# Performance work log

Measured on AMD Instinct MI355X. Metric: run time of the kernel, lower is better.

## Reference

```python
import jax, jax.numpy as jnp
import numpy as np


def _dwconv(x, w, pad, dil=1):
    # x: [B,C,H,W], w: [C,1,kh,kw] depthwise
    C = x.shape[1]
    return jax.lax.conv_general_dilated(
        x, w, window_strides=(1, 1), padding=[(pad, pad), (pad, pad)],
        rhs_dilation=(dil, dil),
        dimension_numbers=('NCHW', 'OIHW', 'NCHW'),
        feature_group_count=C)


def _conv1x1(x, w, b):
    # w: [O,C,1,1]
    return jnp.einsum('bchw,oc->bohw', x, w[:, :, 0, 0]) + b[None, :, None, None]


def _ln(x, g, b, eps=1e-6):
    mu = x.mean(-1, keepdims=True)
    var = ((x - mu) ** 2).mean(-1, keepdims=True)
    return (x - mu) * jax.lax.rsqrt(var + eps) * g + b


def _gelu(x):
    return jax.nn.gelu(x, approximate=False)  # torch nn.GELU default = exact erf


def _starts(h, step, ps):
    s = []
    for i in range(0, h + step - ps, step):
        s.append(i if i + ps <= h else h - ps)
    return np.asarray(s, np.int32)


def _divisor(h, w, step, ps):
    # replicates patch_reverse's overlap /2 strips exactly
    div = np.ones((h, w), np.float32)
    for i in range(step, h + step - ps, step):
        top, down = i, i + ps - step
        if top + ps > h:
            top = h - ps
        div[top:down, :] *= 2.0
    for j in range(step, w + step - ps, step):
        left, right = j, j + ps - step
        if left + ps > w:
            left = w - ps
        div[:, left:right] *= 2.0
    return div


def _forward(x, ps, lth_dw_w, lth_pw_w, lth_pw_b, lth_gate_w, lth_gate_b, lth_scale,
             ln1_g, ln1_b, ln2_g, ln2_b, qkv_w, gate_w, gate_b, proj_w, pe_w, pe_b,
             fc1_w, fc1_b, dw_w, dw_b, fc2_w, fc2_b):
    B, C, H, W = x.shape
    step = ps - 2
    # ---- Low_to_high ----
    low = x.reshape(B, C, H // 2, 2, W // 2, 2).mean(axis=(3, 5))  # adaptive avg pool (even H,W)
    low_up = jax.image.resize(low, (B, C, H, W), method='bilinear')  # align_corners=False
    hf = x - low_up
    sgate = jax.nn.sigmoid(_conv1x1(jnp.abs(hf), lth_gate_w, lth_gate_b))  # [B,1,H,W]
    refined = _conv1x1(_gelu(_dwconv(hf, lth_dw_w, pad=2, dil=2)), lth_pw_w, lth_pw_b)
    x = x + lth_scale * refined * sgate
    # ---- patch_divide (overlapping windows) ----
    st = ps if (H == ps and W == ps) else step
    tops, lefts = _starts(H, st, ps), _starts(W, st, ps)
    nh, nw = len(tops), len(lefts)
    r = tops[:, None] + np.arange(ps)   # [nh, ps]
    c = lefts[:, None] + np.arange(ps)  # [nw, ps]
    crop = x[:, :, r[:, None, :, None], c[None, :, None, :]]  # [B,C,nh,nw,ps,ps]
    t = crop.transpose(0, 2, 3, 4, 5, 1).reshape(B * nh * nw, ps * ps, C)  # (b n) (h w) c
    # ---- Attention (single-head, qk_dim == dim) ----
    y = _ln(t, ln1_g, ln1_b)
    qkv = y @ qkv_w                      # [Bn, N, 3C]
    q, k, v = jnp.split(qkv, 3, axis=-1)
    z = _gelu(y @ gate_w + gate_b)       # gate
    qimg = q.transpose(0, 2, 1).reshape(-1, C, ps, ps)
    pe = (_dwconv(qimg, pe_w, pad=1) + pe_b[None, :, None, None])
    pe = pe.reshape(-1, C, ps * ps).transpose(0, 2, 1)
    scale = C ** (-0.5)                  # qk_dim = dim = C
    attn = jax.nn.softmax(jnp.einsum('bnc,bmc->bnm', q, k) * scale, axis=-1)
    out = jnp.einsum('bnm,bmc->bnc', attn, v) + pe
    t = (out * z) @ proj_w + t           # proj + residual
    # ---- patch_reverse (overlap-add, strips averaged) ----
    crop = t.reshape(B, nh, nw, ps, ps, C).transpose(0, 5, 1, 2, 3, 4)  # [B,C,nh,nw,ps,ps]
    summed = jnp.zeros_like(x).at[:, :, r[:, None, :, None], c[None, :, None, :]].add(crop)
    x = summed * (1.0 / jnp.asarray(_divisor(H, W, st, ps)))
    # ---- ConvFFN ----
    xt = x.reshape(B, C, H * W).transpose(0, 2, 1)  # [B,HW,C]
    y = _ln(xt, ln2_g, ln2_b)
    y = _gelu(y @ fc1_w + fc1_b)                    # [B,HW,2C]
    yimg = y.transpose(0, 2, 1).reshape(B, -1, H, W)
    y = y + (_dwconv(yimg, dw_w, pad=2) + dw_b[None, :, None, None]).reshape(B, -1, H * W).transpose(0, 2, 1)
    y = y @ fc2_w + fc2_b
    xt = y + xt
    return xt.transpose(0, 2, 1).reshape(B, C, H, W)


def setup_inputs() -> dict:
    key = jax.random.key(0)
    ks = jax.random.split(key, 16)
    B, C, H, W = 8, 128, 128, 128
    HID = 2 * C
    def w(i, shape, s=0.02):
        return jax.random.normal(ks[i], shape, jnp.float32) * s
    return {
        'x': jax.random.normal(ks[0], (B, C, H, W), jnp.float32),
        'ps': 16,
        'lth_dw_w': w(1, (C, 1, 3, 3), 0.1),
        'lth_pw_w': w(2, (C, C, 1, 1)),
        'lth_pw_b': jnp.zeros((C,), jnp.float32),
        'lth_gate_w': w(3, (1, C, 1, 1), 0.1),
        'lth_gate_b': jnp.zeros((1,), jnp.float32),
        'lth_scale': w(4, (1, C, 1, 1), 0.1),
        'ln1_g': jnp.ones((C,), jnp.float32),
        'ln1_b': jnp.zeros((C,), jnp.float32),
        'ln2_g': jnp.ones((C,), jnp.float32),
        'ln2_b': jnp.zeros((C,), jnp.float32),
        'qkv_w': w(5, (C, 3 * C)),
        'gate_w': w(6, (C, C)),
        'gate_b': jnp.zeros((C,), jnp.float32),
        'proj_w': w(7, (C, C)),
        'pe_w': w(8, (C, 1, 3, 3), 0.1),
        'pe_b': jnp.zeros((C,), jnp.float32),
        'fc1_w': w(9, (C, HID)),
        'fc1_b': jnp.zeros((HID,), jnp.float32),
        'dw_w': w(10, (HID, 1, 5, 5), 0.1),
        'dw_b': jnp.zeros((HID,), jnp.float32),
        'fc2_w': w(11, (HID, C)),
        'fc2_b': jnp.zeros((C,), jnp.float32),
    }


def reference(x, ps, lth_dw_w, lth_pw_w, lth_pw_b, lth_gate_w, lth_gate_b, lth_scale,
              ln1_g, ln1_b, ln2_g, ln2_b, qkv_w, gate_w, gate_b, proj_w, pe_w, pe_b,
              fc1_w, fc1_b, dw_w, dw_b, fc2_w, fc2_b):
    return _forward(x, ps, lth_dw_w, lth_pw_w, lth_pw_b, lth_gate_w, lth_gate_b, lth_scale,
                    ln1_g, ln1_b, ln2_g, ln2_b, qkv_w, gate_w, gate_b, proj_w, pe_w, pe_b,
                    fc1_w, fc1_b, dw_w, dw_b, fc2_w, fc2_b)
```

## Files before the change

### kernel.cpp

```cpp
#include <hip/hip_runtime.h>
#include <hip/hip_bf16.h>
#include <math.h>

typedef __hip_bfloat16 bf16;
typedef __attribute__((ext_vector_type(8))) short bf16x8;
typedef __attribute__((ext_vector_type(4))) float f32x4;

static constexpr int B_ = 8, C_ = 128, H_ = 128, W_ = 128;
static constexpr int N_ = H_ * W_;
static constexpr int NWIN = 648;

__device__ __forceinline__ float b2f(bf16 v) { return __bfloat162float(v); }
__device__ __forceinline__ bf16 f2b(float v) { return __float2bfloat16(v); }

__device__ __forceinline__ float gelu_f(float x) {
    float xs = x * 0.70710678118654752f;
    float ax = fabsf(xs);
    float t = 1.0f / fmaf(0.3275911f, ax, 1.0f);
    float poly = t * fmaf(t, fmaf(t, fmaf(t, fmaf(t, 1.061405429f, -1.453152027f), 1.421413741f), -0.284496736f), 0.254829592f);
    float erf_ax = fmaf(-poly, __expf(-ax * ax), 1.0f);
    float erfv = copysignf(erf_ax, xs);
    return 0.5f * x * (1.0f + erfv);
}

__device__ __forceinline__ void load_row12(const char* tile, int a, int wg, float* dst) {
    int base = a * 288 + wg * 16;
    union { uint4 u; bf16 hh[8]; } c0, c1, c2;
    c0.u = *(const uint4*)(tile + base);
    c1.u = *(const uint4*)(tile + base + 16);
    c2.u = *(const uint4*)(tile + base + 32);
    dst[0] = b2f(c0.hh[6]); dst[1] = b2f(c0.hh[7]);
    #pragma unroll
    for (int j = 0; j < 8; ++j) dst[2 + j] = b2f(c1.hh[j]);
    dst[10] = b2f(c2.hh[0]); dst[11] = b2f(c2.hh[1]);
}

__global__ __launch_bounds__(256) void k_wprep(const float* __restrict__ projw, const float* __restrict__ qkvw,
                                               const float* __restrict__ gatew, const float* __restrict__ w1,
                                               const float* __restrict__ w2, const float* __restrict__ pww,
                                               bf16* __restrict__ wt, bf16* __restrict__ wqkv,
                                               bf16* __restrict__ wt1, bf16* __restrict__ wt2,
                                               bf16* __restrict__ wpw) {
    int idx = blockIdx.x * 256 + threadIdx.x;
    if (idx < 16384) {
        int o = idx >> 7, c = idx & 127;
        wt[idx] = f2b(projw[c * 128 + o]);
    } else if (idx < 81920) {
        int i = idx - 16384; int o = i >> 7, c = i & 127;
        wqkv[i] = f2b((o < 384) ? qkvw[c * 384 + o] : gatew[c * 128 + (o - 384)]);
    } else if (idx < 114688) {
        int i = idx - 81920; int o = i >> 7, c = i & 127;
        wt1[i] = f2b(w1[c * 256 + o]);
    } else if (idx < 147456) {
        int i = idx - 114688; int o = i >> 8, c = i & 255;
        wt2[i] = f2b(w2[c * 128 + o]);
    } else {
        int i = idx - 147456;
        wpw[i] = f2b(pww[i]);
    }
}

__global__ __launch_bounds__(256) void k_hf2(const float* __restrict__ x, bf16* __restrict__ hf) {
    __shared__ float lowt[10][64];
    int tid = threadIdx.x;
    int bid = blockIdx.x;
    int ht = bid & 7, c = (bid >> 3) & 127, b = bid >> 10;
    const float* xp = x + (size_t)(b * C_ + c) * N_;
    int h0 = ht * 16;
    int lo0 = (h0 >> 1) - 1;
    for (int e = tid; e < 640; e += 256) {
        int lr = e >> 6, jc = e & 63;
        int j = lo0 + lr; j = j < 0 ? 0 : (j > 63 ? 63 : j);
        const float* pr = xp + (2 * j) * W_ + 2 * jc;
        lowt[lr][jc] = (pr[0] + pr[1] + pr[W_] + pr[W_ + 1]) * 0.25f;
    }
    __syncthreads();
    int hl = tid >> 4, wg = tid & 15;
    int h = h0 + hl;
    int jh = h >> 1;
    int j0, j1; float wh0, wh1;
    if (h & 1) { j0 = jh; j1 = jh + 1 > 63 ? 63 : jh + 1; wh0 = 0.75f; wh1 = 0.25f; }
    else       { j0 = jh - 1 < 0 ? 0 : jh - 1; j1 = jh;   wh0 = 0.25f; wh1 = 0.75f; }
    int l0 = j0 - lo0, l1 = j1 - lo0;
    float4 xa = *(const float4*)(xp + h * W_ + wg * 8);
    float4 xb = *(const float4*)(xp + h * W_ + wg * 8 + 4);
    float xv[8] = {xa.x, xa.y, xa.z, xa.w, xb.x, xb.y, xb.z, xb.w};
    union { bf16 hh[8]; uint4 u; } outv;
    #pragma unroll
    for (int k2 = 0; k2 < 8; ++k2) {
        int w = wg * 8 + k2;
        int jw = w >> 1;
        int w0, w1; float ww0, ww1;
        if (w & 1) { w0 = jw; w1 = jw + 1 > 63 ? 63 : jw + 1; ww0 = 0.75f; ww1 = 0.25f; }
        else       { w0 = jw - 1 < 0 ? 0 : jw - 1; w1 = jw;   ww0 = 0.25f; ww1 = 0.75f; }
        float up = wh0 * (ww0 * lowt[l0][w0] + ww1 * lowt[l0][w1])
                 + wh1 * (ww0 * lowt[l1][w0] + ww1 * lowt[l1][w1]);
        outv.hh[k2] = f2b(xv[k2] - up);
    }
    *(uint4*)(hf + (size_t)(b * C_ + c) * N_ + h * W_ + wg * 8) = outv.u;
}

__global__ __launch_bounds__(256) void k_sgate(const bf16* __restrict__ hf, const float* __restrict__ gw,
                                               const float* __restrict__ gb, float* __restrict__ sg) {
    int idx = blockIdx.x * 256 + threadIdx.x;
    int n = idx & (N_ - 1); int b = idx >> 14;
    const bf16* p = hf + (size_t)b * C_ * N_ + n;
    float s = 0.f;
    for (int c = 0; c < C_; ++c) s += gw[c] * fabsf(b2f(p[(size_t)c * N_]));
    s += gb[0];
    sg[idx] = 1.0f / (1.0f + __expf(-s));
}

__global__ __launch_bounds__(256) void k_dw3p(const bf16* __restrict__ hf, const float* __restrict__ wdw,
                                              bf16* __restrict__ g) {
    __shared__ __align__(16) char tile[38016];
    int tid = threadIdx.x;
    int bid = blockIdx.x;
    int ch = bid & 127, b = bid >> 7;
    const bf16* p = hf + (size_t)(b * C_ + ch) * N_;
    for (int e = tid; e < 2376; e += 256) *(uint4*)(tile + e * 16) = (uint4){0, 0, 0, 0};
    __syncthreads();
    for (int e = tid; e < 2048; e += 256) {
        int gr = e >> 4, slot = e & 15;
        uint4 val = *(const uint4*)(p + gr * 128 + slot * 8);
        *(uint4*)(tile + (gr + 2) * 288 + 16 + slot * 16) = val;
    }
    float kw[9];
    #pragma unroll
    for (int j = 0; j < 9; ++j) kw[j] = wdw[ch * 9 + j];
    __syncthreads();
    int hg = tid >> 4, wg = tid & 15;
    int h0 = hg * 8;
    float ring[5][12];
    #pragma unroll
    for (int j = 0; j < 4; ++j) load_row12(tile, h0 + j, wg, ring[j]);
    bf16* op = g + (size_t)(b * C_ + ch) * N_;
    #pragma unroll
    for (int rr = 0; rr < 8; ++rr) {
        load_row12(tile, h0 + rr + 4, wg, ring[(rr + 4) % 5]);
        float acc[8] = {};
        #pragma unroll
        for (int ky = 0; ky < 3; ++ky) {
            const float* e = ring[(rr + 2 * ky) % 5];
            #pragma unroll
            for (int ow = 0; ow < 8; ++ow) {
                acc[ow] = fmaf(kw[ky * 3 + 0], e[ow], acc[ow]);
                acc[ow] = fmaf(kw[ky * 3 + 1], e[ow + 2], acc[ow]);
                acc[ow] = fmaf(kw[ky * 3 + 2], e[ow + 4], acc[ow]);
            }
        }
        union { bf16 h[8]; uint4 u; } outv;
        #pragma unroll
        for (int ow = 0; ow < 8; ++ow) outv.h[ow] = f2b(gelu_f(acc[ow]));
        *(uint4*)(op + (h0 + rr) * 128 + wg * 8) = outv.u;
    }
}

__global__ __launch_bounds__(256) void k_pw_mfma(const bf16* __restrict__ g, const bf16* __restrict__ wpw,
                                                 const float* __restrict__ pwb, const float* __restrict__ x,
                                                 const float* __restrict__ scale, const float* __restrict__ sg,
                                                 bf16* __restrict__ x1) {
    __shared__ __align__(16) char lds[49152];
    int tid = threadIdx.x;
    int lane = tid & 63, w = tid >> 6;
    int l15 = lane & 15, lhi = lane >> 4;
    int gtok = blockIdx.x * 64; int b = gtok >> 14; int nb = gtok & (N_ - 1);
    char* wch = lds + 16384;
    for (int e = tid; e < 8192; e += 256) {
        int c = e >> 6, i = e & 63;
        bf16 val = g[(size_t)(b * C_ + c) * N_ + nb + i];
        *(bf16*)(lds + i * 256 + ((2 * c) ^ ((i & 7) << 4))) = val;
    }
    for (int e = tid; e < 2048; e += 256) {
        int row = e >> 4, slot = e & 15;
        uint4 val = *(const uint4*)((const char*)wpw + row * 256 + slot * 16);
        *(uint4*)(wch + row * 256 + ((slot * 16) ^ ((row & 7) << 4))) = val;
    }
    __syncthreads();
    bf16x8 afr[4];
    {
        int row = w * 16 + l15;
        #pragma unroll
        for (int cc = 0; cc < 4; ++cc) {
            int cbyt = cc * 64 + lhi * 16;
            afr[cc] = *(const bf16x8*)(lds + row * 256 + (cbyt ^ ((row & 7) << 4)));
        }
    }
    f32x4 acc[8];
    #pragma unroll
    for (int t = 0; t < 8; ++t) acc[t] = (f32x4){0.f, 0.f, 0.f, 0.f};
    #pragma unroll
    for (int ot = 0; ot < 8; ++ot) {
        int row = ot * 16 + l15;
        #pragma unroll
        for (int cc = 0; cc < 4; ++cc) {
            int cbyt = cc * 64 + lhi * 16;
            bf16x8 bfr = *(const bf16x8*)(wch + row * 256 + (cbyt ^ ((row & 7) << 4)));
            acc[ot] = __builtin_amdgcn_mfma_f32_16x16x32_bf16(afr[cc], bfr, acc[ot], 0, 0, 0);
        }
    }
    int n0 = nb + w * 16 + lhi * 4;
    float4 sg4 = *(const float4*)&sg[b * N_ + n0];
    #pragma unroll
    for (int ot = 0; ot < 8; ++ot) {
        int o = ot * 16 + l15;
        size_t obase = (size_t)(b * C_ + o) * N_ + n0;
        float4 x4 = *(const float4*)&x[obase];
        float sc = scale[o], bi = pwb[o];
        union { bf16 h[4]; uint2 u; } t4;
        t4.h[0] = f2b(x4.x + sc * (acc[ot][0] + bi) * sg4.x);
        t4.h[1] = f2b(x4.y + sc * (acc[ot][1] + bi) * sg4.y);
        t4.h[2] = f2b(x4.z + sc * (acc[ot][2] + bi) * sg4.z);
        t4.h[3] = f2b(x4.w + sc * (acc[ot][3] + bi) * sg4.w);
        *(uint2*)(x1 + obase) = t4.u;
    }
}

__global__ __launch_bounds__(256) void k_qkv_mfma(const bf16* __restrict__ x1, const float* __restrict__ lng,
                                                  const float* __restrict__ lnb, const bf16* __restrict__ wall,
                                                  const float* __restrict__ gateb,
                                                  bf16* __restrict__ q, bf16* __restrict__ k,
                                                  bf16* __restrict__ v, bf16* __restrict__ z) {
    __shared__ __align__(16) char lds[49664];
    __shared__ float red2[8][64];
    __shared__ float mu_l[64], rs_l[64];
    int tid = threadIdx.x;
    int lane = tid & 63, w = tid >> 6;
    int l15 = lane & 15, lhi = lane >> 4;
    int win = blockIdx.x >> 2; int qbase = (blockIdx.x & 3) * 64;
    int b = win / 81; int r0 = win % 81; int top = (r0 / 9) * 14, left = (r0 % 9) * 14;
    float* xf = (float*)(lds + 16384);
    char* wchunk = lds + 16384;
    for (int e = tid; e < 8192; e += 256) {
        int c = e >> 6, i = e & 63; int tok = qbase + i; int p = tok >> 4, qq = tok & 15;
        xf[c * 65 + i] = b2f(x1[(size_t)(b * C_ + c) * N_ + (top + p) * W_ + (left + qq)]);
    }
    __syncthreads();
    {
        int i = tid & 63, r = tid >> 6;
        float s = 0.f, ss = 0.f;
        for (int cc = r * 32; cc < r * 32 + 32; ++cc) { float vv = xf[cc * 65 + i]; s += vv; ss += vv * vv; }
        red2[r][i] = s; red2[4 + r][i] = ss;
    }
    __syncthreads();
    if (tid < 64) {
        float s = red2[0][tid] + red2[1][tid] + red2[2][tid] + red2[3][tid];
        float ss = red2[4][tid] + red2[5][tid] + red2[6][tid] + red2[7][tid];
        float mu = s * (1.f / 128.f); float var = ss * (1.f / 128.f) - mu * mu;
        mu_l[tid] = mu; rs_l[tid] = rsqrtf(var + 1e-6f);
    }
    __syncthreads();
    {
        int c = tid & 127;
        float g = lng[c], be = lnb[c];
        for (int e = tid; e < 8192; e += 256) {
            int i = e >> 7;
            float val = (xf[c * 65 + i] - mu_l[i]) * rs_l[i] * g + be;
            *(bf16*)(lds + i * 256 + ((2 * c) ^ ((i & 7) << 4))) = f2b(val);
        }
    }
    __syncthreads();
    bf16x8 afr[4];
    {
        int row = w * 16 + l15;
        #pragma unroll
        for (int cc = 0; cc < 4; ++cc) {
            int cbyt = cc * 64 + lhi * 16;
            afr[cc] = *(const bf16x8*)(lds + row * 256 + (cbyt ^ ((row & 7) << 4)));
        }
    }
    for (int pass = 0; pass < 4; ++pass) {
        __syncthreads();
        for (int e = tid; e < 2048; e += 256) {
            int row = e >> 4, slot = e & 15;
            uint4 val = *(const uint4*)((const char*)wall + (size_t)(pass * 128 + row) * 256 + slot * 16);
            *(uint4*)(wchunk + row * 256 + ((slot * 16) ^ ((row & 7) << 4))) = val;
        }
        __syncthreads();
        f32x4 acc[8];
        #pragma unroll
        for (int t = 0; t < 8; ++t) acc[t] = (f32x4){0.f, 0.f, 0.f, 0.f};
        #pragma unroll
        for (int ot = 0; ot < 8; ++ot) {
            int row = ot * 16 + l15;
            #pragma unroll
            for (int cc = 0; cc < 4; ++cc) {
                int cbyt = cc * 64 + lhi * 16;
                bf16x8 bfr = *(const bf16x8*)(wchunk + row * 256 + (cbyt ^ ((row & 7) << 4)));
                acc[ot] = __builtin_amdgcn_mfma_f32_16x16x32_bf16(afr[cc], bfr, acc[ot], 0, 0, 0);
            }
        }
        if (pass != 2) {
            bf16* outp = (pass == 0) ? q : (pass == 1) ? k : z;
            bool gel = (pass == 3);
            #pragma unroll
            for (int ot = 0; ot < 8; ++ot) {
                int o = ot * 16 + l15;
                float gb = gel ? gateb[o] : 0.f;
                #pragma unroll
                for (int r = 0; r < 4; ++r) {
                    int gtok = qbase + w * 16 + lhi * 4 + r;
                    float vv = acc[ot][r];
                    outp[((size_t)win * 256 + gtok) * 128 + o] = gel ? f2b(gelu_f(vv + gb)) : f2b(vv);
                }
            }
        } else {
            #pragma unroll
            for (int ot = 0; ot < 8; ++ot) {
                int o = ot * 16 + l15;
                union { bf16 h[4]; uint2 u; } t4;
                #pragma unroll
                for (int r = 0; r < 4; ++r) t4.h[r] = f2b(acc[ot][r]);
                *(uint2*)(v + (size_t)win * 32768 + (size_t)o * 256 + qbase + w * 16 + lhi * 4) = t4.u;
            }
        }
    }
}

__global__ __launch_bounds__(256) void k_attn_mfma(const bf16* __restrict__ qb, const bf16* __restrict__ kb,
                                                   const bf16* __restrict__ vb, bf16* __restrict__ ob) {
    __shared__ __align__(16) char lds[49152];
    int tid = threadIdx.x;
    int lane = tid & 63, w = tid >> 6;
    int l15 = lane & 15, lhi = lane >> 4;
    int win = blockIdx.x >> 2, qbase = (blockIdx.x & 3) * 64;
    const bf16* qg = qb + ((size_t)win * 256 + qbase) * 128;
    const bf16* kg = kb + (size_t)win * 256 * 128;
    const bf16* vg = vb + (size_t)win * 128 * 256;
    char* chunk = lds + 32768;
    for (int e = tid; e < 1024; e += 256) {
        int row = e >> 4, slot = e & 15;
        uint4 val = *(const uint4*)((const char*)qg + row * 256 + slot * 16);
        *(uint4*)(lds + row * 256 + ((slot * 16) ^ ((row & 7) << 4))) = val;
    }
    __syncthreads();
    bf16x8 afr[4];
    {
        int row = w * 16 + l15;
        #pragma unroll
        for (int cc = 0; cc < 4; ++cc) {
            int cb = cc * 64 + lhi * 16;
            afr[cc] = *(const bf16x8*)(lds + row * 256 + (cb ^ ((row & 7) << 4)));
        }
    }
    f32x4 acc[16];
    #pragma unroll
    for (int t = 0; t < 16; ++t) acc[t] = (f32x4){0.f, 0.f, 0.f, 0.f};
    for (int kc = 0; kc < 4; ++kc) {
        __syncthreads();
        for (int e = tid; e < 1024; e += 256) {
            int row = e >> 4, slot = e & 15;
            uint4 val = *(const uint4*)((const char*)kg + (size_t)(kc * 64 + row) * 256 + slot * 16);
            *(uint4*)(chunk + row * 256 + ((slot * 16) ^ ((row & 7) << 4))) = val;
        }
        __syncthreads();
        #pragma unroll
        for (int t = 0; t < 4; ++t) {
            int row = t * 16 + l15;
            #pragma unroll
            for (int cc = 0; cc < 4; ++cc) {
                int cb = cc * 64 + lhi * 16;
                bf16x8 bfr = *(const bf16x8*)(chunk + row * 256 + (cb ^ ((row & 7) << 4)));
                acc[kc * 4 + t] = __builtin_amdgcn_mfma_f32_16x16x32_bf16(afr[cc], bfr, acc[kc * 4 + t], 0, 0, 0);
            }
        }
    }
    const float sm_scale = 0.08838834764831845f;
    #pragma unroll
    for (int r = 0; r < 4; ++r) {
        float m = -1e30f;
        #pragma unroll
        for (int t = 0; t < 16; ++t) m = fmaxf(m, acc[t][r]);
        #pragma unroll
        for (int d2 = 1; d2 < 16; d2 <<= 1) m = fmaxf(m, __shfl_xor(m, d2, 64));
        float ssum = 0.f;
        #pragma unroll
        for (int t = 0; t < 16; ++t) { float p = __expf((acc[t][r] - m) * sm_scale); acc[t][r] = p; ssum += p; }
        #pragma unroll
        for (int d2 = 1; d2 < 16; d2 <<= 1) ssum += __shfl_xor(ssum, d2, 64);
        float inv = 1.f / ssum;
        #pragma unroll
        for (int t = 0; t < 16; ++t) acc[t][r] *= inv;
    }
    #pragma unroll
    for (int t = 0; t < 16; ++t) {
        #pragma unroll
        for (int r = 0; r < 4; ++r) {
            int row = w * 16 + lhi * 4 + r;
            int cb = (t * 16 + l15) * 2;
            *(bf16*)(lds + row * 512 + (cb ^ ((row & 7) << 4))) = f2b(acc[t][r]);
        }
    }
    f32x4 oacc[8];
    #pragma unroll
    for (int t = 0; t < 8; ++t) oacc[t] = (f32x4){0.f, 0.f, 0.f, 0.f};
    for (int vc = 0; vc < 4; ++vc) {
        __syncthreads();
        for (int e = tid; e < 1024; e += 256) {
            int row = e >> 3, slot = e & 7;
            uint4 val = *(const uint4*)((const char*)vg + (size_t)row * 512 + vc * 128 + slot * 16);
            *(uint4*)(chunk + row * 128 + ((slot * 16) ^ ((row & 7) << 4))) = val;
        }
        __syncthreads();
        #pragma unroll
        for (int jc = 0; jc < 2; ++jc) {
            int prow = w * 16 + l15;
            int pcb = vc * 128 + jc * 64 + lhi * 16;
            bf16x8 ap = *(const bf16x8*)(lds + prow * 512 + (pcb ^ ((prow & 7) << 4)));
            #pragma unroll
            for (int ct = 0; ct < 8; ++ct) {
                int vrow = ct * 16 + l15;
                int vcb = jc * 64 + lhi * 16;
                bf16x8 bv = *(const bf16x8*)(chunk + vrow * 128 + (vcb ^ ((vrow & 7) << 4)));
                oacc[ct] = __builtin_amdgcn_mfma_f32_16x16x32_bf16(ap, bv, oacc[ct], 0, 0, 0);
            }
        }
    }
    bf16* og = ob + ((size_t)win * 256 + qbase) * 128;
    #pragma unroll
    for (int ct = 0; ct < 8; ++ct) {
        #pragma unroll
        for (int r = 0; r < 4; ++r) {
            int row = w * 16 + lhi * 4 + r;
            og[row * 128 + ct * 16 + l15] = f2b(oacc[ct][r]);
        }
    }
}

__global__ __launch_bounds__(256) void k_peg(bf16* __restrict__ ob, const bf16* __restrict__ qb,
                                             const bf16* __restrict__ zb,
                                             const float* __restrict__ pew, const float* __restrict__ peb) {
    __shared__ float pw_lds[1152];
    __shared__ float pb_lds[128];
    int tid = threadIdx.x;
    for (int e = tid; e < 1152; e += 256) pw_lds[e] = pew[e];
    if (tid < 128) pb_lds[tid] = peb[tid];
    __syncthreads();
    int g = blockIdx.x * 256 + tid;
    int c8 = g & 15, tok = (g >> 4) & 255, win = g >> 12;
    int cb = c8 * 8;
    int pp = tok >> 4, qq = tok & 15;
    size_t base = ((size_t)win * 256 + tok) * 128 + cb;
    float pv[8];
    #pragma unroll
    for (int cc = 0; cc < 8; ++cc) pv[cc] = pb_lds[cb + cc];
    #pragma unroll
    for (int ky = 0; ky < 3; ++ky) {
        int py = pp + ky - 1; if ((unsigned)py >= 16u) continue;
        #pragma unroll
        for (int kx = 0; kx < 3; ++kx) {
            int qx = qq + kx - 1; if ((unsigned)qx >= 16u) continue;
            union { uint4 u; bf16 h[8]; } qu;
            qu.u = *(const uint4*)(qb + ((size_t)win * 256 + py * 16 + qx) * 128 + cb);
            #pragma unroll
            for (int cc = 0; cc < 8; ++cc)
                pv[cc] += pw_lds[(cb + cc) * 9 + ky * 3 + kx] * b2f(qu.h[cc]);
        }
    }
    union { uint4 u; bf16 h[8]; } ou, zu, ru;
    ou.u = *(const uint4*)(ob + base);
    zu.u = *(const uint4*)(zb + base);
    #pragma unroll
    for (int cc = 0; cc < 8; ++cc)
        ru.h[cc] = f2b((b2f(ou.h[cc]) + pv[cc]) * b2f(zu.h[cc]));
    *(uint4*)(ob + base) = ru.u;
}

__global__ __launch_bounds__(256) void k_proj(const bf16* __restrict__ ub, const bf16* __restrict__ wt,
                                              const bf16* __restrict__ x1, bf16* __restrict__ t2) {
    __shared__ __align__(16) char lds[49152];
    int tid = threadIdx.x;
    int lane = tid & 63, w = tid >> 6;
    int l15 = lane & 15, lhi = lane >> 4;
    int win = blockIdx.x >> 2, qbase = (blockIdx.x & 3) * 64;
    int b = win / 81; int r0 = win % 81; int top = (r0 / 9) * 14, left = (r0 % 9) * 14;
    const bf16* ug = ub + ((size_t)win * 256 + qbase) * 128;
    char* wchunk = lds + 16384;
    for (int e = tid; e < 1024; e += 256) {
        int row = e >> 4, slot = e & 15;
        uint4 val = *(const uint4*)((const char*)ug + row * 256 + slot * 16);
        *(uint4*)(lds + row * 256 + ((slot * 16) ^ ((row & 7) << 4))) = val;
    }
    for (int e = tid; e < 2048; e += 256) {
        int row = e >> 4, slot = e & 15;
        uint4 val = *(const uint4*)((const char*)wt + row * 256 + slot * 16);
        *(uint4*)(wchunk + row * 256 + ((slot * 16) ^ ((row & 7) << 4))) = val;
    }
    __syncthreads();
    bf16x8 afr[4];
    {
        int row = w * 16 + l15;
        #pragma unroll
        for (int cc = 0; cc < 4; ++cc) {
            int cbyt = cc * 64 + lhi * 16;
            afr[cc] = *(const bf16x8*)(lds + row * 256 + (cbyt ^ ((row & 7) << 4)));
        }
    }
    f32x4 acc[8];
    #pragma unroll
    for (int t = 0; t < 8; ++t) acc[t] = (f32x4){0.f, 0.f, 0.f, 0.f};
    #pragma unroll
    for (int ot = 0; ot < 8; ++ot) {
        int row = ot * 16 + l15;
        #pragma unroll
        for (int cc = 0; cc < 4; ++cc) {
            int cbyt = cc * 64 + lhi * 16;
            bf16x8 bfr = *(const bf16x8*)(wchunk + row * 256 + (cbyt ^ ((row & 7) << 4)));
            acc[ot] = __builtin_amdgcn_mfma_f32_16x16x32_bf16(afr[cc], bfr, acc[ot], 0, 0, 0);
        }
    }
    #pragma unroll
    for (int ot = 0; ot < 8; ++ot) {
        #pragma unroll
        for (int r = 0; r < 4; ++r) {
            int tok = w * 16 + lhi * 4 + r;
            int o = ot * 16 + l15;
            int gtok = qbase + tok;
            int p = gtok >> 4, qq = gtok & 15;
            float res = b2f(x1[(size_t)(b * C_ + o) * N_ + (top + p) * W_ + (left + qq)]);
            t2[(size_t)win * 32768 + (size_t)o * 256 + gtok] = f2b(acc[ot][r] + res);
        }
    }
}

__global__ __launch_bounds__(256) void k_fc1ln(const bf16* __restrict__ t2, const float* __restrict__ lng,
                                               const float* __restrict__ lnb, const bf16* __restrict__ wt1,
                                               const float* __restrict__ b1, bf16* __restrict__ h1,
                                               bf16* __restrict__ x2w) {
    __shared__ __align__(16) char lds[49664];
    __shared__ float red2[8][64];
    __shared__ float mu_l[64], rs_l[64];
    int tid = threadIdx.x;
    int lane = tid & 63, w = tid >> 6;
    int l15 = lane & 15, lhi = lane >> 4;
    int gtok = blockIdx.x * 64; int b = gtok >> 14; int nb = gtok & (N_ - 1);
    int h = nb >> 7, w0 = nb & 127;
    int imin = (h < 16) ? 0 : (h - 2) / 14; int imax = h / 14; if (imax > 8) imax = 8;
    int jmin0 = (w0 < 16) ? 0 : (w0 - 2) / 14;
    int jmax0 = (w0 + 63) / 14; if (jmax0 > 8) jmax0 = 8;
    float* xf = (float*)(lds + 16384);
    char* wch = lds + 16384;
    for (int e = tid; e < 8320; e += 256) xf[e] = 0.f;
    __syncthreads();
    {
        int c = tid >> 1, half = tid & 1;
        for (int ii = imin; ii <= imax; ++ii) {
            int trow = h - ii * 14;
            for (int jj = jmin0; jj <= jmax0; ++jj) {
                int s = jj * 14 - w0 + half * 8;
                if (s >= 0 && s <= 56) {
                    const bf16* tp = t2 + (size_t)((b * 9 + ii) * 9 + jj) * 32768
                                   + (size_t)c * 256 + trow * 16 + half * 8;
                    union { uint4 u; bf16 hh[8]; } qv;
                    qv.u = *(const uint4*)tp;
                    float* xr = xf + c * 65 + s;
                    #pragma unroll
                    for (int k2 = 0; k2 < 8; ++k2) xr[k2] += b2f(qv.hh[k2]);
                }
            }
        }
    }
    __syncthreads();
    for (int e = tid; e < 2048; e += 256) {
        int c = e >> 4, qd = e & 15;
        int i0 = qd * 4;
        union { bf16 hh[4]; uint2 u; } t4;
        #pragma unroll
        for (int k2 = 0; k2 < 4; ++k2) {
            int i = i0 + k2;
            int wp = w0 + i;
            int jmn = (wp < 16) ? 0 : (wp - 2) / 14; int jmx = wp / 14; if (jmx > 8) jmx = 8;
            float inv = 1.0f / (float)((imax - imin + 1) * (jmx - jmn + 1));
            float val = xf[c * 65 + i] * inv;
            xf[c * 65 + i] = val;
            t4.hh[k2] = f2b(val);
        }
        *(uint2*)(x2w + (size_t)(b * C_ + c) * N_ + nb + i0) = t4.u;
    }
    __syncthreads();
    {
        int i = tid & 63, r = tid >> 6;
        float s = 0.f, ss = 0.f;
        for (int cc = r * 32; cc < r * 32 + 32; ++cc) { float vv = xf[cc * 65 + i]; s += vv; ss += vv * vv; }
        red2[r][i] = s; red2[4 + r][i] = ss;
    }
    __syncthreads();
    if (tid < 64) {
        float s = red2[0][tid] + red2[1][tid] + red2[2][tid] + red2[3][tid];
        float ss = red2[4][tid] + red2[5][tid] + red2[6][tid] + red2[7][tid];
        float mu = s * (1.f / 128.f); float var = ss * (1.f / 128.f) - mu * mu;
        mu_l[tid] = mu; rs_l[tid] = rsqrtf(var + 1e-6f);
    }
    __syncthreads();
    {
        int c = tid & 127;
        float g = lng[c], be = lnb[c];
        for (int e = tid; e < 8192; e += 256) {
            int i = e >> 7;
            float val = (xf[c * 65 + i] - mu_l[i]) * rs_l[i] * g + be;
            *(bf16*)(lds + i * 256 + ((2 * c) ^ ((i & 7) << 4))) = f2b(val);
        }
    }
    __syncthreads();
    bf16x8 afr[4];
    {
        int row = w * 16 + l15;
        #pragma unroll
        for (int cc = 0; cc < 4; ++cc) {
            int cbyt = cc * 64 + lhi * 16;
            afr[cc] = *(const bf16x8*)(lds + row * 256 + (cbyt ^ ((row & 7) << 4)));
        }
    }
    for (int p = 0; p < 2; ++p) {
        __syncthreads();
        for (int e = tid; e < 2048; e += 256) {
            int row = e >> 4, slot = e & 15;
            uint4 val = *(const uint4*)((const char*)wt1 + (size_t)(p * 128 + row) * 256 + slot * 16);
            *(uint4*)(wch + row * 256 + ((slot * 16) ^ ((row & 7) << 4))) = val;
        }
        __syncthreads();
        f32x4 acc[8];
        #pragma unroll
        for (int t = 0; t < 8; ++t) acc[t] = (f32x4){0.f, 0.f, 0.f, 0.f};
        #pragma unroll
        for (int ot = 0; ot < 8; ++ot) {
            int row = ot * 16 + l15;
            #pragma unroll
            for (int cc = 0; cc < 4; ++cc) {
                int cbyt = cc * 64 + lhi * 16;
                bf16x8 bfr = *(const bf16x8*)(wch + row * 256 + (cbyt ^ ((row & 7) << 4)));
                acc[ot] = __builtin_amdgcn_mfma_f32_16x16x32_bf16(afr[cc], bfr, acc[ot], 0, 0, 0);
            }
        }
        int n0 = nb + w * 16 + lhi * 4;
        #pragma unroll
        for (int ot = 0; ot < 8; ++ot) {
            int o = p * 128 + ot * 16 + l15;
            float bi = b1[o];
            union { bf16 h[4]; uint2 u; } t4;
            #pragma unroll
            for (int r = 0; r < 4; ++r) t4.h[r] = f2b(gelu_f(acc[ot][r] + bi));
            *(uint2*)(h1 + (size_t)(b * 256 + o) * N_ + n0) = t4.u;
        }
    }
}

__global__ __launch_bounds__(256) void k_dw5p(const bf16* __restrict__ h1, const float* __restrict__ wdw,
                                              const float* __restrict__ bdw, bf16* __restrict__ h2) {
    __shared__ __align__(16) char tile[38016];
    int tid = threadIdx.x;
    int bid = blockIdx.x;
    int ch = bid & 255, b = bid >> 8;
    const bf16* p = h1 + (size_t)(b * 256 + ch) * N_;
    for (int e = tid; e < 2376; e += 256) *(uint4*)(tile + e * 16) = (uint4){0, 0, 0, 0};
    __syncthreads();
    for (int e = tid; e < 2048; e += 256) {
        int gr = e >> 4, slot = e & 15;
        uint4 val = *(const uint4*)(p + gr * 128 + slot * 8);
        *(uint4*)(tile + (gr + 2) * 288 + 16 + slot * 16) = val;
    }
    float kw[25];
    #pragma unroll
    for (int j = 0; j < 25; ++j) kw[j] = wdw[ch * 25 + j];
    float bi = bdw[ch];
    __syncthreads();
    int hg = tid >> 4, wg = tid & 15;
    int h0 = hg * 8;
    float ring[5][12];
    #pragma unroll
    for (int j = 0; j < 4; ++j) load_row12(tile, h0 + j, wg, ring[j]);
    bf16* op = h2 + (size_t)(b * 256 + ch) * N_;
    #pragma unroll
    for (int rr = 0; rr < 8; ++rr) {
        load_row12(tile, h0 + rr + 4, wg, ring[(rr + 4) % 5]);
        float acc[8];
        #pragma unroll
        for (int ow = 0; ow < 8; ++ow) acc[ow] = bi;
        #pragma unroll
        for (int ky = 0; ky < 5; ++ky) {
            const float* e = ring[(rr + ky) % 5];
            #pragma unroll
            for (int ow = 0; ow < 8; ++ow) {
                #pragma unroll
                for (int kx = 0; kx < 5; ++kx)
                    acc[ow] = fmaf(kw[ky * 5 + kx], e[ow + kx], acc[ow]);
            }
        }
        {
            const float* e = ring[(rr + 2) % 5];
            #pragma unroll
            for (int ow = 0; ow < 8; ++ow) acc[ow] += e[ow + 2];
        }
        union { bf16 h[8]; uint4 u; } outv;
        #pragma unroll
        for (int ow = 0; ow < 8; ++ow) outv.h[ow] = f2b(acc[ow]);
        *(uint4*)(op + (h0 + rr) * 128 + wg * 8) = outv.u;
    }
}

__global__ __launch_bounds__(256) void k_fc2_mfma(const bf16* __restrict__ h2, const bf16* __restrict__ wt2,
                                                  const float* __restrict__ b2, const bf16* __restrict__ x2,
                                                  float* __restrict__ out) {
    __shared__ __align__(16) char lds[65536];
    int tid = threadIdx.x;
    int lane = tid & 63, w = tid >> 6;
    int l15 = lane & 15, lhi = lane >> 4;
    int gtok = blockIdx.x * 64; int b = gtok >> 14; int nb = gtok & (N_ - 1);
    char* wch = lds + 32768;
    for (int e = tid; e < 16384; e += 256) {
        int c = e >> 6, i = e & 63;
        bf16 val = h2[(size_t)(b * 256 + c) * N_ + nb + i];
        *(bf16*)(lds + i * 512 + ((2 * c) ^ ((i & 7) << 4))) = val;
    }
    __syncthreads();
    bf16x8 afr[8];
    {
        int row = w * 16 + l15;
        #pragma unroll
        for (int cc = 0; cc < 8; ++cc) {
            int cbyt = cc * 64 + lhi * 16;
            afr[cc] = *(const bf16x8*)(lds + row * 512 + (cbyt ^ ((row & 7) << 4)));
        }
    }
    f32x4 acc[8];
    #pragma unroll
    for (int t = 0; t < 8; ++t) acc[t] = (f32x4){0.f, 0.f, 0.f, 0.f};
    for (int kh = 0; kh < 2; ++kh) {
        __syncthreads();
        for (int e = tid; e < 2048; e += 256) {
            int row = e >> 4, slot = e & 15;
            uint4 val = *(const uint4*)((const char*)wt2 + (size_t)row * 512 + kh * 256 + slot * 16);
            *(uint4*)(wch + row * 256 + ((slot * 16) ^ ((row & 7) << 4))) = val;
        }
        __syncthreads();
        #pragma unroll
        for (int ot = 0; ot < 8; ++ot) {
            int row = ot * 16 + l15;
            #pragma unroll
            for (int cc = 0; cc < 4; ++cc) {
                int cbyt = cc * 64 + lhi * 16;
                bf16x8 bfr = *(const bf16x8*)(wch + row * 256 + (cbyt ^ ((row & 7) << 4)));
                acc[ot] = __builtin_amdgcn_mfma_f32_16x16x32_bf16(afr[kh * 4 + cc], bfr, acc[ot], 0, 0, 0);
            }
        }
    }
    int n0 = nb + w * 16 + lhi * 4;
    #pragma unroll
    for (int ot = 0; ot < 8; ++ot) {
        int o = ot * 16 + l15;
        size_t obase = (size_t)(b * C_ + o) * N_ + n0;
        float bi = b2[o];
        union { uint2 u; bf16 h[4]; } xr;
        xr.u = *(const uint2*)(x2 + obase);
        float4 r4;
        r4.x = acc[ot][0] + bi + b2f(xr.h[0]);
        r4.y = acc[ot][1] + bi + b2f(xr.h[1]);
        r4.z = acc[ot][2] + bi + b2f(xr.h[2]);
        r4.w = acc[ot][3] + bi + b2f(xr.h[3]);
        *(float4*)(out + obase) = r4;
    }
}

extern "C" void kernel_launch(void* const* d_in, const int* in_sizes, int n_in,
                              void* d_out, int out_size, void* d_ws, size_t ws_size,
                              hipStream_t stream) {
    const float* x         = (const float*)d_in[0];
    const float* lth_dw_w  = (const float*)d_in[2];
    const float* lth_pw_w  = (const float*)d_in[3];
    const float* lth_pw_b  = (const float*)d_in[4];
    const float* lth_gate_w= (const float*)d_in[5];
    const float* lth_gate_b= (const float*)d_in[6];
    const float* lth_scale = (const float*)d_in[7];
    const float* ln1_g     = (const float*)d_in[8];
    const float* ln1_b     = (const float*)d_in[9];
    const float* ln2_g     = (const float*)d_in[10];
    const float* ln2_b     = (const float*)d_in[11];
    const float* qkv_w     = (const float*)d_in[12];
    const float* gate_w    = (const float*)d_in[13];
    const float* gate_b    = (const float*)d_in[14];
    const float* proj_w    = (const float*)d_in[15];
    const float* pe_w      = (const float*)d_in[16];
    const float* pe_b      = (const float*)d_in[17];
    const float* fc1_w     = (const float*)d_in[18];
    const float* fc1_b     = (const float*)d_in[19];
    const float* dw_w      = (const float*)d_in[20];
    const float* dw_b      = (const float*)d_in[21];
    const float* fc2_w     = (const float*)d_in[22];
    const float* fc2_b     = (const float*)d_in[23];

    char* ws = (char*)d_ws;
    constexpr size_t SZ_X = 33554432;
    constexpr size_t SZ_W = 42467328;
    constexpr size_t OFF_A = 0;
    constexpr size_t OFF_B = OFF_A + SZ_X;
    constexpr size_t OFF_C = OFF_B + SZ_W;
    constexpr size_t OFF_D = OFF_C + SZ_W;
    constexpr size_t OFF_E = OFF_D + SZ_W;
    constexpr size_t OFF_F = OFF_E + SZ_W;
    constexpr size_t OFF_G = OFF_F + SZ_W;
    constexpr size_t OFF_H = OFF_G + 32768;
    constexpr size_t OFF_I = OFF_H + 131072;

    bf16*  x1  = (bf16*)(ws + OFF_A);
    bf16*  h2  = (bf16*)(ws + OFF_A);
    float* sg  = (float*)(ws + OFF_B + 16777216);
    bf16*  o   = (bf16*)(ws + OFF_B);
    bf16*  q   = (bf16*)(ws + OFF_C);
    bf16*  x2  = (bf16*)(ws + OFF_C);
    bf16*  hf  = (bf16*)(ws + OFF_D);
    bf16*  k   = (bf16*)(ws + OFF_D);
    bf16*  t2  = (bf16*)(ws + OFF_D);
    bf16*  g   = (bf16*)(ws + OFF_E);
    bf16*  v   = (bf16*)(ws + OFF_E);
    bf16*  h1  = (bf16*)(ws + OFF_E);
    bf16*  z   = (bf16*)(ws + OFF_F);
    bf16*  wt  = (bf16*)(ws + OFF_G);
    bf16*  wqkv= (bf16*)(ws + OFF_H);
    bf16*  wt1 = (bf16*)(ws + OFF_I);
    bf16*  wt2 = (bf16*)(ws + OFF_I + 65536);
    bf16*  wpw = (bf16*)(ws + OFF_I + 131072);

    k_wprep   <<<640,   256, 0, stream>>>(proj_w, qkv_w, gate_w, fc1_w, fc2_w, lth_pw_w,
                                          wt, wqkv, wt1, wt2, wpw);
    k_hf2     <<<8192,  256, 0, stream>>>(x, hf);
    k_sgate   <<<512,   256, 0, stream>>>(hf, lth_gate_w, lth_gate_b, sg);
    k_dw3p    <<<1024,  256, 0, stream>>>(hf, lth_dw_w, g);
    k_pw_mfma <<<2048,  256, 0, stream>>>(g, wpw, lth_pw_b, x, lth_scale, sg, x1);
    k_qkv_mfma<<<2592,  256, 0, stream>>>(x1, ln1_g, ln1_b, wqkv, gate_b, q, k, v, z);
    k_attn_mfma<<<2592, 256, 0, stream>>>(q, k, v, o);
    k_peg     <<<10368, 256, 0, stream>>>(o, q, z, pe_w, pe_b);
    k_proj    <<<2592,  256, 0, stream>>>(o, wt, x1, t2);
    k_fc1ln   <<<2048,  256, 0, stream>>>(t2, ln2_g, ln2_b, wt1, fc1_b, h1, x2);
    k_dw5p    <<<2048,  256, 0, stream>>>(h1, dw_w, dw_b, h2);
    k_fc2_mfma<<<2048,  256, 0, stream>>>(h2, wt2, fc2_b, x2, (float*)d_out);
}
```

Before: 522.8 us.

## Transpose MFMA operands so epilogue stores are vectorized, remap attention blocks per XCD

The QKV/gate passes swap the MFMA operand roles (weights as A, token fragments as B) so each lane holds four consecutive output channels and can write them with one 8-byte store instead of four scattered 2-byte stores. The attention kernel does the same swap for its PV product and vectorizes its output store. It also remaps block indices so that blocks sharing a window land on the same XCD, for L2 locality. The projection epilogue reads its residual and writes t2 with packed 32-bit and 64-bit accesses. The cost is that all 16 token fragments are held in registers (yfr), which raises register pressure.

```diff
diff --git a/kernel.cpp b/kernel.cpp
--- a/kernel.cpp
+++ b/kernel.cpp
@@ -260,13 +260,14 @@
         }
     }
     __syncthreads();
-    bf16x8 afr[4];
-    {
-        int row = w * 16 + l15;
+    bf16x8 yfr[4][4];
+    #pragma unroll
+    for (int tb = 0; tb < 4; ++tb) {
+        int row = tb * 16 + l15;
         #pragma unroll
         for (int cc = 0; cc < 4; ++cc) {
             int cbyt = cc * 64 + lhi * 16;
-            afr[cc] = *(const bf16x8*)(lds + row * 256 + (cbyt ^ ((row & 7) << 4)));
+            yfr[tb][cc] = *(const bf16x8*)(lds + row * 256 + (cbyt ^ ((row & 7) << 4)));
         }
     }
     for (int pass = 0; pass < 4; ++pass) {
@@ -277,34 +278,68 @@
             *(uint4*)(wchunk + row * 256 + ((slot * 16) ^ ((row & 7) << 4))) = val;
         }
         __syncthreads();
-        f32x4 acc[8];
-        #pragma unroll
-        for (int t = 0; t < 8; ++t) acc[t] = (f32x4){0.f, 0.f, 0.f, 0.f};
-        #pragma unroll
-        for (int ot = 0; ot < 8; ++ot) {
-            int row = ot * 16 + l15;
-            #pragma unroll
-            for (int cc = 0; cc < 4; ++cc) {
-                int cbyt = cc * 64 + lhi * 16;
-                bf16x8 bfr = *(const bf16x8*)(wchunk + row * 256 + (cbyt ^ ((row & 7) << 4)));
-                acc[ot] = __builtin_amdgcn_mfma_f32_16x16x32_bf16(afr[cc], bfr, acc[ot], 0, 0, 0);
-            }
-        }
         if (pass != 2) {
+            bf16x8 wfr[2][4];
+            #pragma unroll
+            for (int mb = 0; mb < 2; ++mb) {
+                int row = w * 32 + mb * 16 + l15;
+                #pragma unroll
+                for (int cc = 0; cc < 4; ++cc) {
+                    int cbyt = cc * 64 + lhi * 16;
+                    wfr[mb][cc] = *(const bf16x8*)(wchunk + row * 256 + (cbyt ^ ((row & 7) << 4)));
+                }
+            }
+            f32x4 acc[8];
+            #pragma unroll
+            for (int t = 0; t < 8; ++t) acc[t] = (f32x4){0.f, 0.f, 0.f, 0.f};
+            #pragma unroll
+            for (int mb = 0; mb < 2; ++mb)
+                #pragma unroll
+                for (int tb = 0; tb < 4; ++tb)
+                    #pragma unroll
+                    for (int cc = 0; cc < 4; ++cc)
+                        acc[mb * 4 + tb] = __builtin_amdgcn_mfma_f32_16x16x32_bf16(
+                            wfr[mb][cc], yfr[tb][cc], acc[mb * 4 + tb], 0, 0, 0);
             bf16* outp = (pass == 0) ? q : (pass == 1) ? k : z;
             bool gel = (pass == 3);
             #pragma unroll
+            for (int mb = 0; mb < 2; ++mb) {
+                int o4 = w * 32 + mb * 16 + lhi * 4;
+                #pragma unroll
+                for (int tb = 0; tb < 4; ++tb) {
+                    int tok = qbase + tb * 16 + l15;
+                    union { bf16 h[4]; uint2 u; } t4;
+                    #pragma unroll
+                    for (int r = 0; r < 4; ++r) {
+                        float vv = acc[mb * 4 + tb][r];
+                        t4.h[r] = gel ? f2b(gelu_f(vv + gateb[o4 + r])) : f2b(vv);
+                    }
+                    *(uint2*)(outp + ((size_t)win * 256 + tok) * 128 + o4) = t4.u;
+                }
+            }
+        } else {
+            bf16x8 afr[4];
+            {
+                int row = w * 16 + l15;
+                #pragma unroll
+                for (int cc = 0; cc < 4; ++cc) {
+                    int cbyt = cc * 64 + lhi * 16;
+                    afr[cc] = *(const bf16x8*)(lds + row * 256 + (cbyt ^ ((row & 7) << 4)));
+                }
+            }
+            f32x4 acc[8];
+            #pragma unroll
+            for (int t = 0; t < 8; ++t) acc[t] = (f32x4){0.f, 0.f, 0.f, 0.f};
+            #pragma unroll
             for (int ot = 0; ot < 8; ++ot) {
-                int o = ot * 16 + l15;
-                float gb = gel ? gateb[o] : 0.f;
+                int row = ot * 16 + l15;
                 #pragma unroll
-                for (int r = 0; r < 4; ++r) {
-                    int gtok = qbase + w * 16 + lhi * 4 + r;
-                    float vv = acc[ot][r];
-                    outp[((size_t)win * 256 + gtok) * 128 + o] = gel ? f2b(gelu_f(vv + gb)) : f2b(vv);
+                for (int cc = 0; cc < 4; ++cc) {
+                    int cbyt = cc * 64 + lhi * 16;
+                    bf16x8 bfr = *(const bf16x8*)(wchunk + row * 256 + (cbyt ^ ((row & 7) << 4)));
+                    acc[ot] = __builtin_amdgcn_mfma_f32_16x16x32_bf16(afr[cc], bfr, acc[ot], 0, 0, 0);
                 }
             }
-        } else {
             #pragma unroll
             for (int ot = 0; ot < 8; ++ot) {
                 int o = ot * 16 + l15;
@@ -323,7 +358,9 @@
     int tid = threadIdx.x;
     int lane = tid & 63, w = tid >> 6;
     int l15 = lane & 15, lhi = lane >> 4;
-    int win = blockIdx.x >> 2, qbase = (blockIdx.x & 3) * 64;
+    int xcd = blockIdx.x & 7, ixd = blockIdx.x >> 3;
+    int win = xcd * 81 + (ixd >> 2);
+    int qbase = (ixd & 3) * 64;
     const bf16* qg = qb + ((size_t)win * 256 + qbase) * 128;
     const bf16* kg = kb + (size_t)win * 256 * 128;
     const bf16* vg = vb + (size_t)win * 128 * 256;
@@ -412,17 +449,20 @@
                 int vrow = ct * 16 + l15;
                 int vcb = jc * 64 + lhi * 16;
                 bf16x8 bv = *(const bf16x8*)(chunk + vrow * 128 + (vcb ^ ((vrow & 7) << 4)));
-                oacc[ct] = __builtin_amdgcn_mfma_f32_16x16x32_bf16(ap, bv, oacc[ct], 0, 0, 0);
+                oacc[ct] = __builtin_amdgcn_mfma_f32_16x16x32_bf16(bv, ap, oacc[ct], 0, 0, 0);
             }
         }
     }
     bf16* og = ob + ((size_t)win * 256 + qbase) * 128;
-    #pragma unroll
-    for (int ct = 0; ct < 8; ++ct) {
-        #pragma unroll
-        for (int r = 0; r < 4; ++r) {
-            int row = w * 16 + lhi * 4 + r;
-            og[row * 128 + ct * 16 + l15] = f2b(oacc[ct][r]);
+    {
+        int tok = w * 16 + l15;
+        #pragma unroll
+        for (int ct = 0; ct < 8; ++ct) {
+            int c4 = ct * 16 + lhi * 4;
+            union { bf16 h[4]; uint2 u; } t4;
+            #pragma unroll
+            for (int r = 0; r < 4; ++r) t4.h[r] = f2b(oacc[ct][r]);
+            *(uint2*)(og + tok * 128 + c4) = t4.u;
         }
     }
 }
@@ -509,17 +549,18 @@
             acc[ot] = __builtin_amdgcn_mfma_f32_16x16x32_bf16(afr[cc], bfr, acc[ot], 0, 0, 0);
         }
     }
+    int gtok0 = qbase + w * 16 + lhi * 4;
+    int p = gtok0 >> 4, qq = gtok0 & 15;
     #pragma unroll
     for (int ot = 0; ot < 8; ++ot) {
-        #pragma unroll
-        for (int r = 0; r < 4; ++r) {
-            int tok = w * 16 + lhi * 4 + r;
-            int o = ot * 16 + l15;
-            int gtok = qbase + tok;
-            int p = gtok >> 4, qq = gtok & 15;
-            float res = b2f(x1[(size_t)(b * C_ + o) * N_ + (top + p) * W_ + (left + qq)]);
-            t2[(size_t)win * 32768 + (size_t)o * 256 + gtok] = f2b(acc[ot][r] + res);
-        }
+        int o = ot * 16 + l15;
+        const uint* xr32 = (const uint*)(x1 + (size_t)(b * C_ + o) * N_ + (top + p) * W_ + left + qq);
+        union { uint u2[2]; bf16 h[4]; } xv;
+        xv.u2[0] = xr32[0]; xv.u2[1] = xr32[1];
+        union { bf16 h[4]; uint2 u; } t4;
+        #pragma unroll
+        for (int r = 0; r < 4; ++r) t4.h[r] = f2b(acc[ot][r] + b2f(xv.h[r]));
+        *(uint2*)(t2 + (size_t)win * 32768 + (size_t)o * 256 + gtok0) = t4.u;
     }
 }
 
```

After: 544.3 us. +4.1%, slower.
